# Kernel tuning notes

Hardware: AMD Instinct MI355X
Metric: run time of the kernel (lower is better)

## Reference

```python
import jax, jax.numpy as jnp
import numpy as np

C_CT, C_MRI, C_OUT = 64, 64, 64
B, D, H, W = 1, 8, 32, 32


def setup_inputs() -> dict:
    key = jax.random.key(0)
    ks = jax.random.split(key, 18)
    s = 0.05
    inp = {
        "ct_features": jax.random.normal(ks[0], (B, C_CT, D, H, W), jnp.float32),
        "mri_features": jax.random.normal(ks[1], (B, C_MRI, D, H, W), jnp.float32),
        # 1x1x1 Conv3d == per-voxel linear: weight (out, in), bias (out,)
        "wq_ct": jax.random.normal(ks[2], (C_OUT, C_CT), jnp.float32) * s,
        "bq_ct": jax.random.normal(ks[3], (C_OUT,), jnp.float32) * s,
        "wk_mri": jax.random.normal(ks[4], (C_OUT, C_MRI), jnp.float32) * s,
        "bk_mri": jax.random.normal(ks[5], (C_OUT,), jnp.float32) * s,
        "wv_mri": jax.random.normal(ks[6], (C_OUT, C_MRI), jnp.float32) * s,
        "bv_mri": jax.random.normal(ks[7], (C_OUT,), jnp.float32) * s,
        "wq_mri": jax.random.normal(ks[8], (C_OUT, C_MRI), jnp.float32) * s,
        "bq_mri": jax.random.normal(ks[9], (C_OUT,), jnp.float32) * s,
        "wk_ct": jax.random.normal(ks[10], (C_OUT, C_CT), jnp.float32) * s,
        "bk_ct": jax.random.normal(ks[11], (C_OUT,), jnp.float32) * s,
        "wv_ct": jax.random.normal(ks[12], (C_OUT, C_CT), jnp.float32) * s,
        "bv_ct": jax.random.normal(ks[13], (C_OUT,), jnp.float32) * s,
        "wo": jax.random.normal(ks[14], (C_OUT, 2 * C_OUT), jnp.float32) * s,
        "bo": jax.random.normal(ks[15], (C_OUT,), jnp.float32) * s,
    }
    return inp


def _proj(x_flat, w, b):
    # x_flat: (B, Cin, N); 1x1x1 conv -> (B, Cout, N)
    return jnp.einsum("oc,bcn->bon", w, x_flat) + b[None, :, None]


def _forward(ct, mri, wq_ct, bq_ct, wk_mri, bk_mri, wv_mri, bv_mri,
             wq_mri, bq_mri, wk_ct, bk_ct, wv_ct, bv_ct, wo, bo):
    b, _, d, h, w = ct.shape
    n = d * h * w
    ct_f = ct.reshape(b, ct.shape[1], n)
    mri_f = mri.reshape(b, mri.shape[1], n)
    scale = 1.0 / np.sqrt(C_OUT).astype(np.float32)

    # CT queries attend over MRI keys/values
    ct_q = _proj(ct_f, wq_ct, bq_ct)      # (B, C, N)
    mri_k = _proj(mri_f, wk_mri, bk_mri)  # (B, C, N)
    mri_v = _proj(mri_f, wv_mri, bv_mri)  # (B, C, N)
    attn_ct = jax.nn.softmax(jnp.einsum("bci,bcj->bij", ct_q, mri_k) * scale, axis=-1)
    ct_att = jnp.einsum("bcj,bij->bci", mri_v, attn_ct)  # (B, C, N)

    # MRI queries attend over CT keys/values
    mri_q = _proj(mri_f, wq_mri, bq_mri)
    ct_k = _proj(ct_f, wk_ct, bk_ct)
    ct_v = _proj(ct_f, wv_ct, bv_ct)
    attn_mri = jax.nn.softmax(jnp.einsum("bci,bcj->bij", mri_q, ct_k) * scale, axis=-1)
    mri_att = jnp.einsum("bcj,bij->bci", ct_v, attn_mri)

    fused = jnp.concatenate([ct_att, mri_att], axis=1)  # (B, 2C, N)
    out = _proj(fused, wo, bo)  # (B, C, N)
    return out.reshape(b, C_OUT, d, h, w)


def reference(ct_features, mri_features, wq_ct, bq_ct, wk_mri, bk_mri,
              wv_mri, bv_mri, wq_mri, bq_mri, wk_ct, bk_ct, wv_ct, bv_ct,
              wo, bo):
    return _forward(ct_features, mri_features, wq_ct, bq_ct, wk_mri, bk_mri,
                    wv_mri, bv_mri, wq_mri, bq_mri, wk_ct, bk_ct,
                    wv_ct, bv_ct, wo, bo)
```

## Files before the change

kernel.cpp:

```cpp
#include <hip/hip_runtime.h>
#include <stdint.h>

constexpr int N = 8192;
constexpr float QSCALE = 0.18033688011112042f;
constexpr int SPLIT = 4;

typedef __attribute__((ext_vector_type(4))) float f32x4;
typedef __attribute__((ext_vector_type(4))) unsigned int u32x4;
typedef __attribute__((ext_vector_type(2))) unsigned int u32x2;
typedef __attribute__((ext_vector_type(4))) unsigned short u16x4;

__device__ inline unsigned short f2bf(float f) {
  unsigned u = __builtin_bit_cast(unsigned, f);
  u += 0x7FFFu + ((u >> 16) & 1u);
  return (unsigned short)(u >> 16);
}
__device__ inline float bf2f(unsigned short u) {
  return __builtin_bit_cast(float, (unsigned)u << 16);
}
__device__ inline unsigned cvtpk(float a, float b) {
  unsigned r;
  asm("v_cvt_pk_bf16_f32 %0, %1, %2" : "=v"(r) : "v"(a), "v"(b));
  return r;
}

__device__ inline void mfma16x16x32bf16(f32x4& d, u32x4 a, u32x4 b) {
  asm volatile("v_mfma_f32_16x16x32_bf16 %0, %1, %2, %0" : "+v"(d) : "v"(a), "v"(b));
}
__device__ inline void mfma_guard() {
  __builtin_amdgcn_sched_barrier(0);
  asm volatile("s_nop 7\n\ts_nop 7");
  __builtin_amdgcn_sched_barrier(0);
}
__device__ inline void gload16(const void* src, void* lds) {
  __builtin_amdgcn_global_load_lds(
      (const __attribute__((address_space(1))) unsigned int*)src,
      (__attribute__((address_space(3))) unsigned int*)lds, 16, 0, 0);
}

struct ProjArgs {
  const float* x[6];
  const float* w[6];
  const float* b[6];
  unsigned short* o[6];
  int mode[6];
  float scale[6];
};

__global__ __launch_bounds__(256) void proj_kernel(ProjArgs A) {
  const int p = blockIdx.y;
  const float* __restrict__ x = A.x[p];
  const float* __restrict__ w = A.w[p];
  const float* __restrict__ bias = A.b[p];
  unsigned short* __restrict__ out = A.o[p];
  const int n0 = blockIdx.x * 64;
  __shared__ float Xs[64][64];
  __shared__ float Ws[64][64];
  const int t = threadIdx.x;
#pragma unroll
  for (int i = 0; i < 4; i++) {
    int s = t + i * 256;
    ((u32x4*)Ws)[s] = ((const u32x4*)w)[s];
  }
#pragma unroll
  for (int i = 0; i < 4; i++) {
    int s = t + i * 256;
    int c = s >> 4, nc = s & 15;
    *(u32x4*)&Xs[c][nc * 4] = *(const u32x4*)&x[c * N + n0 + nc * 4];
  }
  __syncthreads();
  const int n = t & 63, h = t >> 6;
  float acc[16];
#pragma unroll
  for (int o = 0; o < 16; o++) acc[o] = bias[h * 16 + o];
  for (int c = 0; c < 64; c++) {
    float xv = Xs[c][n];
#pragma unroll
    for (int o = 0; o < 16; o++) acc[o] = fmaf(Ws[h * 16 + o][c], xv, acc[o]);
  }
  const float sc = A.scale[p];
  if (A.mode[p] == 0) {
    unsigned short* po = out + (size_t)(n0 + n) * 64 + h * 16;
#pragma unroll
    for (int o = 0; o < 16; o++) po[o] = f2bf(acc[o] * sc);
  } else {
#pragma unroll
    for (int o = 0; o < 16; o++) out[(size_t)(h * 16 + o) * N + n0 + n] = f2bf(acc[o] * sc);
  }
}

__global__ __launch_bounds__(256, 4) void attn_kernel(
    const unsigned short* __restrict__ Q0, const unsigned short* __restrict__ K0,
    const unsigned short* __restrict__ V0, const unsigned short* __restrict__ Q1,
    const unsigned short* __restrict__ K1, const unsigned short* __restrict__ V1,
    unsigned short* __restrict__ Opart, float* __restrict__ Lsum) {
  const int bid = blockIdx.x;
  const int slice = bid & 7;
  const int qb = bid >> 3;
  const int dir = slice >> 2;
  const int chunk = slice & 3;
  const unsigned short* __restrict__ Q = dir ? Q1 : Q0;
  const unsigned short* __restrict__ K = dir ? K1 : K0;
  const unsigned short* __restrict__ V = dir ? V1 : V0;

  __shared__ char smem[38912];

  const int t = threadIdx.x;
  const int lane = t & 63, w = t >> 6;
  const int qsub = w >> 1, cw = w & 1;
  const int g = lane >> 4, sl = lane & 15;
  char* const pw = smem + 32768 + w * 1280;
  const int kvbase = chunk * 2048;

  const int srowoff = lane >> 3;
  const int swzb = ((lane & 7) ^ (lane >> 3)) * 16;
  const char* const Kc = (const char*)K;
  const char* const Vc = (const char*)V;

  u32x4 qf[2][2];
#pragma unroll
  for (int rb = 0; rb < 2; rb++) {
    const int qrow = qb * 64 + qsub * 32 + rb * 16 + sl;
#pragma unroll
    for (int ks = 0; ks < 2; ks++)
      qf[rb][ks] = *(const u32x4*)(Q + (size_t)qrow * 64 + ks * 32 + 8 * g);
  }

  f32x4 acc[4][2];
#pragma unroll
  for (int mb = 0; mb < 4; mb++)
#pragma unroll
    for (int rb = 0; rb < 2; rb++)
#pragma unroll
      for (int r = 0; r < 4; r++) acc[mb][rb][r] = 0.f;
  float lpart[2] = {0.f, 0.f};

#pragma unroll
  for (int i = 0; i < 2; i++) {
    const int row = (w * 2 + i) * 8 + srowoff;
    gload16(Kc + (size_t)(kvbase + row) * 128 + swzb,
            smem + (w * 2 + i) * 1024);
    gload16(Vc + (size_t)row * (N * 2) + (size_t)kvbase * 2 + swzb,
            smem + 16384 + (w * 2 + i) * 1024);
  }

  for (int jt = 0; jt < 32; ++jt) {
    asm volatile("s_waitcnt vmcnt(0)" ::: "memory");
    __builtin_amdgcn_s_barrier();
    __builtin_amdgcn_sched_barrier(0);
    const int cur = jt & 1;

    if (jt + 1 < 32) {
      const int j0n = kvbase + (jt + 1) * 64;
      const int nb = cur ^ 1;
#pragma unroll
      for (int i = 0; i < 2; i++) {
        const int row = (w * 2 + i) * 8 + srowoff;
        gload16(Kc + (size_t)(j0n + row) * 128 + swzb,
                smem + nb * 8192 + (w * 2 + i) * 1024);
        gload16(Vc + (size_t)row * (N * 2) + (size_t)j0n * 2 + swzb,
                smem + 16384 + nb * 8192 + (w * 2 + i) * 1024);
      }
    }
    char* const Kl = smem + cur * 8192;
    char* const Vl = smem + 16384 + cur * 8192;

    u32x4 kf[2][2];
#pragma unroll
    for (int jb = 0; jb < 2; jb++) {
      const int row = cw * 32 + jb * 16 + sl;
      const int rs = (row & 7) << 4;
#pragma unroll
      for (int ks = 0; ks < 2; ks++)
        kf[jb][ks] = *(const u32x4*)(Kl + row * 128 + ((ks * 64 + 16 * g) ^ rs));
    }

    f32x4 st[2][2];
    __builtin_amdgcn_s_setprio(1);
#pragma unroll
    for (int jb = 0; jb < 2; jb++)
#pragma unroll
      for (int rb = 0; rb < 2; rb++) {
#pragma unroll
        for (int r = 0; r < 4; r++) st[jb][rb][r] = 0.f;
        mfma16x16x32bf16(st[jb][rb], kf[jb][0], qf[rb][0]);
        mfma16x16x32bf16(st[jb][rb], kf[jb][1], qf[rb][1]);
      }
    __builtin_amdgcn_s_setprio(0);
    mfma_guard();

    u32x4 vf[4];
#pragma unroll
    for (int mb = 0; mb < 4; mb++) {
      const int row = mb * 16 + sl;
      const int rs = (row & 7) << 4;
      vf[mb] = *(const u32x4*)(Vl + row * 128 + ((cw * 64 + 16 * g) ^ rs));
    }

#pragma unroll
    for (int rb = 0; rb < 2; rb++) {
#pragma unroll
      for (int jb = 0; jb < 2; jb++) {
        float e0 = __builtin_amdgcn_exp2f(st[jb][rb][0]);
        float e1 = __builtin_amdgcn_exp2f(st[jb][rb][1]);
        float e2 = __builtin_amdgcn_exp2f(st[jb][rb][2]);
        float e3 = __builtin_amdgcn_exp2f(st[jb][rb][3]);
        lpart[rb] += (e0 + e1) + (e2 + e3);
        u32x2 pk;
        pk[0] = cvtpk(e0, e1);
        pk[1] = cvtpk(e2, e3);
        *(u32x2*)(pw + sl * 80 + jb * 32 + 8 * g) = pk;
      }
      u32x4 pf = *(const u32x4*)(pw + sl * 80 + 16 * g);
      __builtin_amdgcn_s_setprio(1);
#pragma unroll
      for (int mb = 0; mb < 4; mb++)
        mfma16x16x32bf16(acc[mb][rb], vf[mb], pf);
      __builtin_amdgcn_s_setprio(0);
    }
  }
  mfma_guard();

#pragma unroll
  for (int rb = 0; rb < 2; rb++) {
    lpart[rb] += __shfl_xor(lpart[rb], 16);
    lpart[rb] += __shfl_xor(lpart[rb], 32);
  }

  __syncthreads();
  char* const obuf = smem + qsub * 8192;
  float* const mlb = (float*)(smem + 32768);
  if (cw == 1) {
#pragma unroll
    for (int rb = 0; rb < 2; rb++) {
      const int q = rb * 16 + sl;
      const int qswz = (q & 7) << 4;
#pragma unroll
      for (int mb = 0; mb < 4; mb++)
        *(f32x4*)(obuf + q * 256 + (((mb * 16 + 4 * g) * 4) ^ qswz)) = acc[mb][rb];
      if (g == 0) mlb[qsub * 32 + q] = lpart[rb];
    }
  }
  __syncthreads();
  if (cw == 0) {
#pragma unroll
    for (int rb = 0; rb < 2; rb++) {
      const int q = rb * 16 + sl;
      const int qswz = (q & 7) << 4;
      const float ltot = lpart[rb] + mlb[qsub * 32 + q];
      const int qg = qb * 64 + qsub * 32 + q;
      const size_t pbase = ((size_t)slice * N + qg) * 64;
#pragma unroll
      for (int mb = 0; mb < 4; mb++) {
        f32x4 oo = *(const f32x4*)(obuf + q * 256 + (((mb * 16 + 4 * g) * 4) ^ qswz));
        u32x2 pk;
        pk[0] = cvtpk(acc[mb][rb][0] + oo[0], acc[mb][rb][1] + oo[1]);
        pk[1] = cvtpk(acc[mb][rb][2] + oo[2], acc[mb][rb][3] + oo[3]);
        *(u32x2*)(Opart + pbase + mb * 16 + 4 * g) = pk;
      }
      if (g == 0) Lsum[(size_t)slice * N + qg] = ltot;
    }
  }
}

__global__ __launch_bounds__(256) void oproj_kernel(
    const unsigned short* __restrict__ Opart, const float* __restrict__ Lsum,
    const float* __restrict__ wo, const float* __restrict__ bo,
    float* __restrict__ out) {
  __shared__ float Fs[128][32];
  __shared__ float Ws[64][128];
  const int t = threadIdx.x;
  const int n0 = blockIdx.x * 32;
#pragma unroll
  for (int i = 0; i < 8; i++) {
    int s = t + i * 256;
    ((u32x4*)Ws)[s] = ((const u32x4*)wo)[s];
  }
  const int q = t & 31;
  const int cg = t >> 5;
#pragma unroll
  for (int dir = 0; dir < 2; dir++) {
    float lt = 0.f;
#pragma unroll
    for (int c = 0; c < 4; c++) lt += Lsum[(size_t)(dir * SPLIT + c) * N + n0 + q];
    const float rD = 1.0f / lt;
#pragma unroll
    for (int i = 0; i < 2; i++) {
      const int ch4 = cg * 2 + i;
      float s0 = 0.f, s1 = 0.f, s2 = 0.f, s3 = 0.f;
#pragma unroll
      for (int c = 0; c < 4; c++) {
        u16x4 v = *(const u16x4*)(Opart +
            ((size_t)(dir * SPLIT + c) * N + n0 + q) * 64 + ch4 * 4);
        s0 += bf2f(v[0]); s1 += bf2f(v[1]); s2 += bf2f(v[2]); s3 += bf2f(v[3]);
      }
      Fs[dir * 64 + ch4 * 4 + 0][q] = s0 * rD;
      Fs[dir * 64 + ch4 * 4 + 1][q] = s1 * rD;
      Fs[dir * 64 + ch4 * 4 + 2][q] = s2 * rD;
      Fs[dir * 64 + ch4 * 4 + 3][q] = s3 * rD;
    }
  }
  __syncthreads();
  const int n = t & 31, h = t >> 5;
  float acc[8];
#pragma unroll
  for (int o = 0; o < 8; o++) acc[o] = bo[h * 8 + o];
  for (int ch = 0; ch < 128; ch++) {
    float fv = Fs[ch][n];
#pragma unroll
    for (int o = 0; o < 8; o++) acc[o] = fmaf(Ws[h * 8 + o][ch], fv, acc[o]);
  }
#pragma unroll
  for (int o = 0; o < 8; o++) out[(size_t)(h * 8 + o) * N + n0 + n] = acc[o];
}

extern "C" void kernel_launch(void* const* d_in, const int* in_sizes, int n_in,
                              void* d_out, int out_size, void* d_ws, size_t ws_size,
                              hipStream_t stream) {
  const float* ct     = (const float*)d_in[0];
  const float* mri    = (const float*)d_in[1];
  const float* wq_ct  = (const float*)d_in[2];
  const float* bq_ct  = (const float*)d_in[3];
  const float* wk_mri = (const float*)d_in[4];
  const float* bk_mri = (const float*)d_in[5];
  const float* wv_mri = (const float*)d_in[6];
  const float* bv_mri = (const float*)d_in[7];
  const float* wq_mri = (const float*)d_in[8];
  const float* bq_mri = (const float*)d_in[9];
  const float* wk_ct  = (const float*)d_in[10];
  const float* bk_ct  = (const float*)d_in[11];
  const float* wv_ct  = (const float*)d_in[12];
  const float* bv_ct  = (const float*)d_in[13];
  const float* wo     = (const float*)d_in[14];
  const float* bo     = (const float*)d_in[15];

  char* ws = (char*)d_ws;
  const size_t MB = (size_t)1 << 20;
  unsigned short* Qt_ct  = (unsigned short*)(ws + 0 * MB);
  unsigned short* Kt_mri = (unsigned short*)(ws + 1 * MB);
  unsigned short* V_mri  = (unsigned short*)(ws + 2 * MB);
  unsigned short* Qt_mri = (unsigned short*)(ws + 3 * MB);
  unsigned short* Kt_ct  = (unsigned short*)(ws + 4 * MB);
  unsigned short* V_ct   = (unsigned short*)(ws + 5 * MB);
  unsigned short* Opart  = (unsigned short*)(ws + 6 * MB);
  float* Lsum            = (float*)(ws + 14 * MB);

  ProjArgs A;
  A.x[0] = ct;  A.w[0] = wq_ct;  A.b[0] = bq_ct;  A.o[0] = Qt_ct;  A.mode[0] = 0; A.scale[0] = QSCALE;
  A.x[1] = mri; A.w[1] = wk_mri; A.b[1] = bk_mri; A.o[1] = Kt_mri; A.mode[1] = 0; A.scale[1] = 1.f;
  A.x[2] = mri; A.w[2] = wv_mri; A.b[2] = bv_mri; A.o[2] = V_mri;  A.mode[2] = 1; A.scale[2] = 1.f;
  A.x[3] = mri; A.w[3] = wq_mri; A.b[3] = bq_mri; A.o[3] = Qt_mri; A.mode[3] = 0; A.scale[3] = QSCALE;
  A.x[4] = ct;  A.w[4] = wk_ct;  A.b[4] = bk_ct;  A.o[4] = Kt_ct;  A.mode[4] = 0; A.scale[4] = 1.f;
  A.x[5] = ct;  A.w[5] = wv_ct;  A.b[5] = bv_ct;  A.o[5] = V_ct;   A.mode[5] = 1; A.scale[5] = 1.f;

  proj_kernel<<<dim3(128, 6), 256, 0, stream>>>(A);
  attn_kernel<<<dim3(1024), 256, 0, stream>>>(Qt_ct, Kt_mri, V_mri,
                                              Qt_mri, Kt_ct, V_ct, Opart, Lsum);
  oproj_kernel<<<dim3(256), 256, 0, stream>>>(Opart, Lsum, wo, bo, (float*)d_out);
}
```

Before: 75.56 us.

## Software-pipeline QK of next tile with softmax-PV of current tile

Restructures the attention inner loop so the QK^T MFMAs for tile j+1 are issued alongside the exp/PV work for tile j, using ping-pong score and V-fragment registers and a two-ahead LDS prefetch. The aim is to overlap MFMA and transcendental/LDS work within a wave rather than serializing them. Holding the extra live registers forces lowering the occupancy hint from 4 to 3 waves per SIMD, which may reduce latency hiding across waves.

```diff
diff --git a/kernel.cpp b/kernel.cpp
--- a/kernel.cpp
+++ b/kernel.cpp
@@ -89,7 +89,7 @@
   }
 }
 
-__global__ __launch_bounds__(256, 4) void attn_kernel(
+__global__ __launch_bounds__(256, 3) void attn_kernel(
     const unsigned short* __restrict__ Q0, const unsigned short* __restrict__ K0,
     const unsigned short* __restrict__ V0, const unsigned short* __restrict__ Q1,
     const unsigned short* __restrict__ K1, const unsigned short* __restrict__ V1,
@@ -117,6 +117,18 @@
   const char* const Kc = (const char*)K;
   const char* const Vc = (const char*)V;
 
+  auto STAGE = [&](int jtile, int slot) {
+    const int j0 = kvbase + jtile * 64;
+#pragma unroll
+    for (int i = 0; i < 2; i++) {
+      const int row = (w * 2 + i) * 8 + srowoff;
+      gload16(Kc + (size_t)(j0 + row) * 128 + swzb,
+              smem + slot * 8192 + (w * 2 + i) * 1024);
+      gload16(Vc + (size_t)row * (N * 2) + (size_t)j0 * 2 + swzb,
+              smem + 16384 + slot * 8192 + (w * 2 + i) * 1024);
+    }
+  };
+
   u32x4 qf[2][2];
 #pragma unroll
   for (int rb = 0; rb < 2; rb++) {
@@ -135,37 +147,9 @@
       for (int r = 0; r < 4; r++) acc[mb][rb][r] = 0.f;
   float lpart[2] = {0.f, 0.f};
 
-#pragma unroll
-  for (int i = 0; i < 2; i++) {
-    const int row = (w * 2 + i) * 8 + srowoff;
-    gload16(Kc + (size_t)(kvbase + row) * 128 + swzb,
-            smem + (w * 2 + i) * 1024);
-    gload16(Vc + (size_t)row * (N * 2) + (size_t)kvbase * 2 + swzb,
-            smem + 16384 + (w * 2 + i) * 1024);
-  }
-
-  for (int jt = 0; jt < 32; ++jt) {
-    asm volatile("s_waitcnt vmcnt(0)" ::: "memory");
-    __builtin_amdgcn_s_barrier();
-    __builtin_amdgcn_sched_barrier(0);
-    const int cur = jt & 1;
-
-    if (jt + 1 < 32) {
-      const int j0n = kvbase + (jt + 1) * 64;
-      const int nb = cur ^ 1;
-#pragma unroll
-      for (int i = 0; i < 2; i++) {
-        const int row = (w * 2 + i) * 8 + srowoff;
-        gload16(Kc + (size_t)(j0n + row) * 128 + swzb,
-                smem + nb * 8192 + (w * 2 + i) * 1024);
-        gload16(Vc + (size_t)row * (N * 2) + (size_t)j0n * 2 + swzb,
-                smem + 16384 + nb * 8192 + (w * 2 + i) * 1024);
-      }
-    }
-    char* const Kl = smem + cur * 8192;
-    char* const Vl = smem + 16384 + cur * 8192;
-
-    u32x4 kf[2][2];
+  auto READKV = [&](int slot, u32x4 (&kf)[2][2], u32x4 (&vf)[4]) {
+    char* const Kl = smem + slot * 8192;
+    char* const Vl = smem + 16384 + slot * 8192;
 #pragma unroll
     for (int jb = 0; jb < 2; jb++) {
       const int row = cw * 32 + jb * 16 + sl;
@@ -174,8 +158,15 @@
       for (int ks = 0; ks < 2; ks++)
         kf[jb][ks] = *(const u32x4*)(Kl + row * 128 + ((ks * 64 + 16 * g) ^ rs));
     }
-
-    f32x4 st[2][2];
+#pragma unroll
+    for (int mb = 0; mb < 4; mb++) {
+      const int row = mb * 16 + sl;
+      const int rs = (row & 7) << 4;
+      vf[mb] = *(const u32x4*)(Vl + row * 128 + ((cw * 64 + 16 * g) ^ rs));
+    }
+  };
+
+  auto QK = [&](u32x4 (&kf)[2][2], f32x4 (&st)[2][2]) {
     __builtin_amdgcn_s_setprio(1);
 #pragma unroll
     for (int jb = 0; jb < 2; jb++)
@@ -187,16 +178,9 @@
         mfma16x16x32bf16(st[jb][rb], kf[jb][1], qf[rb][1]);
       }
     __builtin_amdgcn_s_setprio(0);
-    mfma_guard();
-
-    u32x4 vf[4];
-#pragma unroll
-    for (int mb = 0; mb < 4; mb++) {
-      const int row = mb * 16 + sl;
-      const int rs = (row & 7) << 4;
-      vf[mb] = *(const u32x4*)(Vl + row * 128 + ((cw * 64 + 16 * g) ^ rs));
-    }
-
+  };
+
+  auto SMPV = [&](f32x4 (&st)[2][2], u32x4 (&vf)[4]) {
 #pragma unroll
     for (int rb = 0; rb < 2; rb++) {
 #pragma unroll
@@ -218,7 +202,39 @@
         mfma16x16x32bf16(acc[mb][rb], vf[mb], pf);
       __builtin_amdgcn_s_setprio(0);
     }
-  }
+  };
+
+  auto STEPF = [&](f32x4 (&stN)[2][2], f32x4 (&stO)[2][2],
+                   u32x4 (&vfN)[4], u32x4 (&vfO)[4], int jt) {
+    asm volatile("s_waitcnt vmcnt(0)" ::: "memory");
+    asm volatile("s_waitcnt lgkmcnt(0)" ::: "memory");
+    __builtin_amdgcn_s_barrier();
+    __builtin_amdgcn_sched_barrier(0);
+    u32x4 kf[2][2];
+    READKV((jt + 1) & 1, kf, vfN);
+    if (jt + 2 < 32) STAGE(jt + 2, jt & 1);
+    QK(kf, stN);
+    SMPV(stO, vfO);
+  };
+
+  STAGE(0, 0);
+  STAGE(1, 1);
+  asm volatile("s_waitcnt vmcnt(0)" ::: "memory");
+  __builtin_amdgcn_s_barrier();
+  f32x4 stA[2][2], stB[2][2];
+  u32x4 vfA[4], vfB[4];
+  {
+    u32x4 kf0[2][2];
+    READKV(0, kf0, vfA);
+    QK(kf0, stA);
+  }
+
+  for (int jt = 0; jt < 30; jt += 2) {
+    STEPF(stB, stA, vfB, vfA, jt);
+    STEPF(stA, stB, vfA, vfB, jt + 1);
+  }
+  STEPF(stB, stA, vfB, vfA, 30);
+  SMPV(stB, vfB);
   mfma_guard();
 
 #pragma unroll
```

Result: slower. 88.53 us (+17.2%).

## Double query tile per attention block to reuse staged K/V tiles

Applied to the files above, without the earlier changes.

Each attention block now handles 128 query rows instead of 64, so every wave holds four 16-row query fragments and accumulators. The grid is halved to 512 blocks and each K/V tile loaded into LDS feeds twice as many MFMAs, which cuts global K/V traffic and per-tile barrier overhead. The cost is higher register and LDS use (launch bounds lowered to 2 blocks per SM, LDS grown to 52 KB) and fewer blocks to fill the GPU, so latency hiding may suffer. The prefetch code is also folded into a STAGE macro.

```diff
diff --git a/kernel.cpp b/kernel.cpp
--- a/kernel.cpp
+++ b/kernel.cpp
@@ -89,7 +89,7 @@
   }
 }
 
-__global__ __launch_bounds__(256, 4) void attn_kernel(
+__global__ __launch_bounds__(256, 2) void attn_kernel(
     const unsigned short* __restrict__ Q0, const unsigned short* __restrict__ K0,
     const unsigned short* __restrict__ V0, const unsigned short* __restrict__ Q1,
     const unsigned short* __restrict__ K1, const unsigned short* __restrict__ V1,
@@ -103,13 +103,13 @@
   const unsigned short* __restrict__ K = dir ? K1 : K0;
   const unsigned short* __restrict__ V = dir ? V1 : V0;
 
-  __shared__ char smem[38912];
+  __shared__ char smem[53248];
 
   const int t = threadIdx.x;
   const int lane = t & 63, w = t >> 6;
   const int qsub = w >> 1, cw = w & 1;
   const int g = lane >> 4, sl = lane & 15;
-  char* const pw = smem + 32768 + w * 1280;
+  char* const pw = smem + 32768 + w * 5120;
   const int kvbase = chunk * 2048;
 
   const int srowoff = lane >> 3;
@@ -117,51 +117,43 @@
   const char* const Kc = (const char*)K;
   const char* const Vc = (const char*)V;
 
-  u32x4 qf[2][2];
-#pragma unroll
-  for (int rb = 0; rb < 2; rb++) {
-    const int qrow = qb * 64 + qsub * 32 + rb * 16 + sl;
+#define STAGE(jtile, slot)                                                     \
+  do {                                                                         \
+    const int j0s = kvbase + (jtile) * 64;                                     \
+    _Pragma("unroll") for (int i = 0; i < 2; i++) {                            \
+      const int row = (w * 2 + i) * 8 + srowoff;                               \
+      gload16(Kc + (size_t)(j0s + row) * 128 + swzb,                           \
+              smem + (slot) * 8192 + (w * 2 + i) * 1024);                      \
+      gload16(Vc + (size_t)row * (N * 2) + (size_t)j0s * 2 + swzb,             \
+              smem + 16384 + (slot) * 8192 + (w * 2 + i) * 1024);              \
+    }                                                                          \
+  } while (0)
+
+  u32x4 qf[4][2];
+#pragma unroll
+  for (int rb = 0; rb < 4; rb++) {
+    const int qrow = qb * 128 + qsub * 64 + rb * 16 + sl;
 #pragma unroll
     for (int ks = 0; ks < 2; ks++)
       qf[rb][ks] = *(const u32x4*)(Q + (size_t)qrow * 64 + ks * 32 + 8 * g);
   }
 
-  f32x4 acc[4][2];
+  f32x4 acc[4][4];
 #pragma unroll
   for (int mb = 0; mb < 4; mb++)
 #pragma unroll
-    for (int rb = 0; rb < 2; rb++)
+    for (int rb = 0; rb < 4; rb++)
 #pragma unroll
       for (int r = 0; r < 4; r++) acc[mb][rb][r] = 0.f;
-  float lpart[2] = {0.f, 0.f};
-
-#pragma unroll
-  for (int i = 0; i < 2; i++) {
-    const int row = (w * 2 + i) * 8 + srowoff;
-    gload16(Kc + (size_t)(kvbase + row) * 128 + swzb,
-            smem + (w * 2 + i) * 1024);
-    gload16(Vc + (size_t)row * (N * 2) + (size_t)kvbase * 2 + swzb,
-            smem + 16384 + (w * 2 + i) * 1024);
-  }
-
+  float lpart[4] = {0.f, 0.f, 0.f, 0.f};
+
+  STAGE(0, 0);
   for (int jt = 0; jt < 32; ++jt) {
     asm volatile("s_waitcnt vmcnt(0)" ::: "memory");
     __builtin_amdgcn_s_barrier();
     __builtin_amdgcn_sched_barrier(0);
     const int cur = jt & 1;
-
-    if (jt + 1 < 32) {
-      const int j0n = kvbase + (jt + 1) * 64;
-      const int nb = cur ^ 1;
-#pragma unroll
-      for (int i = 0; i < 2; i++) {
-        const int row = (w * 2 + i) * 8 + srowoff;
-        gload16(Kc + (size_t)(j0n + row) * 128 + swzb,
-                smem + nb * 8192 + (w * 2 + i) * 1024);
-        gload16(Vc + (size_t)row * (N * 2) + (size_t)j0n * 2 + swzb,
-                smem + 16384 + nb * 8192 + (w * 2 + i) * 1024);
-      }
-    }
+    if (jt + 1 < 32) STAGE(jt + 1, cur ^ 1);
     char* const Kl = smem + cur * 8192;
     char* const Vl = smem + 16384 + cur * 8192;
 
@@ -175,12 +167,12 @@
         kf[jb][ks] = *(const u32x4*)(Kl + row * 128 + ((ks * 64 + 16 * g) ^ rs));
     }
 
-    f32x4 st[2][2];
+    f32x4 st[2][4];
     __builtin_amdgcn_s_setprio(1);
 #pragma unroll
     for (int jb = 0; jb < 2; jb++)
 #pragma unroll
-      for (int rb = 0; rb < 2; rb++) {
+      for (int rb = 0; rb < 4; rb++) {
 #pragma unroll
         for (int r = 0; r < 4; r++) st[jb][rb][r] = 0.f;
         mfma16x16x32bf16(st[jb][rb], kf[jb][0], qf[rb][0]);
@@ -198,7 +190,8 @@
     }
 
 #pragma unroll
-    for (int rb = 0; rb < 2; rb++) {
+    for (int rb = 0; rb < 4; rb++) {
+      const int prow = rb * 16 + sl;
 #pragma unroll
       for (int jb = 0; jb < 2; jb++) {
         float e0 = __builtin_amdgcn_exp2f(st[jb][rb][0]);
@@ -209,9 +202,13 @@
         u32x2 pk;
         pk[0] = cvtpk(e0, e1);
         pk[1] = cvtpk(e2, e3);
-        *(u32x2*)(pw + sl * 80 + jb * 32 + 8 * g) = pk;
+        *(u32x2*)(pw + prow * 80 + jb * 32 + 8 * g) = pk;
       }
-      u32x4 pf = *(const u32x4*)(pw + sl * 80 + 16 * g);
+    }
+
+#pragma unroll
+    for (int rb = 0; rb < 4; rb++) {
+      u32x4 pf = *(const u32x4*)(pw + (rb * 16 + sl) * 80 + 16 * g);
       __builtin_amdgcn_s_setprio(1);
 #pragma unroll
       for (int mb = 0; mb < 4; mb++)
@@ -219,36 +216,37 @@
       __builtin_amdgcn_s_setprio(0);
     }
   }
+#undef STAGE
   mfma_guard();
 
 #pragma unroll
-  for (int rb = 0; rb < 2; rb++) {
+  for (int rb = 0; rb < 4; rb++) {
     lpart[rb] += __shfl_xor(lpart[rb], 16);
     lpart[rb] += __shfl_xor(lpart[rb], 32);
   }
 
   __syncthreads();
-  char* const obuf = smem + qsub * 8192;
+  char* const obuf = smem + qsub * 16384;
   float* const mlb = (float*)(smem + 32768);
   if (cw == 1) {
 #pragma unroll
-    for (int rb = 0; rb < 2; rb++) {
+    for (int rb = 0; rb < 4; rb++) {
       const int q = rb * 16 + sl;
       const int qswz = (q & 7) << 4;
 #pragma unroll
       for (int mb = 0; mb < 4; mb++)
         *(f32x4*)(obuf + q * 256 + (((mb * 16 + 4 * g) * 4) ^ qswz)) = acc[mb][rb];
-      if (g == 0) mlb[qsub * 32 + q] = lpart[rb];
+      if (g == 0) mlb[qsub * 64 + q] = lpart[rb];
     }
   }
   __syncthreads();
   if (cw == 0) {
 #pragma unroll
-    for (int rb = 0; rb < 2; rb++) {
+    for (int rb = 0; rb < 4; rb++) {
       const int q = rb * 16 + sl;
       const int qswz = (q & 7) << 4;
-      const float ltot = lpart[rb] + mlb[qsub * 32 + q];
-      const int qg = qb * 64 + qsub * 32 + q;
+      const float ltot = lpart[rb] + mlb[qsub * 64 + q];
+      const int qg = qb * 128 + qsub * 64 + q;
       const size_t pbase = ((size_t)slice * N + qg) * 64;
 #pragma unroll
       for (int mb = 0; mb < 4; mb++) {
@@ -354,7 +352,7 @@
   A.x[5] = ct;  A.w[5] = wv_ct;  A.b[5] = bv_ct;  A.o[5] = V_ct;   A.mode[5] = 1; A.scale[5] = 1.f;
 
   proj_kernel<<<dim3(128, 6), 256, 0, stream>>>(A);
-  attn_kernel<<<dim3(1024), 256, 0, stream>>>(Qt_ct, Kt_mri, V_mri,
-                                              Qt_mri, Kt_ct, V_ct, Opart, Lsum);
+  attn_kernel<<<dim3(512), 256, 0, stream>>>(Qt_ct, Kt_mri, V_mri,
+                                             Qt_mri, Kt_ct, V_ct, Opart, Lsum);
   oproj_kernel<<<dim3(256), 256, 0, stream>>>(Opart, Lsum, wo, bo, (float*)d_out);
 }
```

Result: faster. 73.07 us (-3.3%).
